# Optimization experiments

Measured on AMD Instinct MI355X. Metric: run time of the kernel, lower is better.

The kernel has to match this reference:

```python
import jax, jax.numpy as jnp
import numpy as np

GROUP_SIZE = 64
SCALING = 32.0 / 16.0  # lora_alpha / r


def setup_inputs() -> dict:
    key = jax.random.key(0)
    k = jax.random.split(key, 7)
    B, S, I, O, R = 4, 2048, 4096, 4096, 16
    G = I // GROUP_SIZE
    x = jax.random.normal(k[0], (B, S, I), dtype=jnp.float32)
    W_q = jax.random.randint(k[1], (O, I), 0, 16, dtype=jnp.int32)
    scale = jax.random.uniform(k[2], (O, G), dtype=jnp.float32) * 0.01 + 1e-4
    zero = jax.random.uniform(k[3], (O, G), dtype=jnp.float32) * 8.0
    lora_A = jax.random.normal(k[4], (I, R), dtype=jnp.float32) * 0.02
    lora_B = jax.random.normal(k[5], (R, O), dtype=jnp.float32) * 0.02
    bias = jax.random.normal(k[6], (O,), dtype=jnp.float32) * 0.01
    return {"x": x, "W_q": W_q, "scale": scale, "zero": zero,
            "lora_A": lora_A, "lora_B": lora_B, "bias": bias}


def reference(x, W_q, scale, zero, lora_A, lora_B, bias):
    O, I = W_q.shape
    G = I // GROUP_SIZE
    # HQQ-style group-wise affine dequant: W = (W_q - zero) * scale  -> [O, I]
    Wg = W_q.reshape(O, G, GROUP_SIZE).astype(scale.dtype)
    W = ((Wg - zero[:, :, None]) * scale[:, :, None]).reshape(O, I)
    # base quantized linear: out = x @ W^T
    out = jnp.einsum('bsi,oi->bso', x, W)
    # LoRA low-rank update (dropout is Identity for p=0)
    out = out + (x @ lora_A @ lora_B) * SCALING
    # bias add
    out = out + bias
    return out
```

## Files before the change

kernel.cpp:

```cpp
#include <hip/hip_runtime.h>
#include <hip/hip_bf16.h>
#include <stdint.h>

#define M_DIM 8192
#define N_DIM 4096
#define K_DIM 4096

typedef __attribute__((ext_vector_type(8))) __bf16 bf16x8;
typedef __attribute__((ext_vector_type(4))) float f32x4;

__device__ inline unsigned short f2bf(float f) {
  unsigned u = __builtin_bit_cast(unsigned, f);
  u += 0x7FFF + ((u >> 16) & 1);
  return (unsigned short)(u >> 16);
}

__device__ inline void async_copy16(const void* g, void* l) {
  __builtin_amdgcn_global_load_lds(
      (const __attribute__((address_space(1))) unsigned int*)g,
      (__attribute__((address_space(3))) unsigned int*)l, 16, 0, 0);
}

__global__ __launch_bounds__(256) void prep_kernel(
    const float* __restrict__ x, unsigned short* __restrict__ xb,
    const int* __restrict__ Wq, const float* __restrict__ scale,
    const float* __restrict__ zero, const float* __restrict__ A,
    const float* __restrict__ Bm, unsigned short* __restrict__ Weff) {
  int t = threadIdx.x;
  if (blockIdx.x < 4096) {
    __shared__ float sA[64 * 17];
    __shared__ float sB[16 * 64];
    int bo = blockIdx.x >> 6;
    int bi = blockIdx.x & 63;
    int o0 = bo * 64, i0 = bi * 64;
    for (int j = t; j < 1024; j += 256) sA[(j >> 4) * 17 + (j & 15)] = A[i0 * 16 + j];
    for (int j = t; j < 1024; j += 256) sB[j] = Bm[(j >> 6) * N_DIM + o0 + (j & 63)];
    __syncthreads();
    for (int e = 0; e < 16; ++e) {
      int idx = e * 256 + t;
      int oo = idx >> 6, ii = idx & 63;
      int o = o0 + oo;
      float sc = scale[o * 64 + bi];
      float zp = zero[o * 64 + bi];
      float w = ((float)Wq[(size_t)o * K_DIM + i0 + ii] - zp) * sc;
      float acc = 0.f;
#pragma unroll
      for (int r = 0; r < 16; ++r) acc += sA[ii * 17 + r] * sB[r * 64 + oo];
      w += 2.0f * acc;
      Weff[(size_t)o * K_DIM + i0 + ii] = f2bf(w);
    }
  } else {
    int i = (blockIdx.x - 4096) * 256 + t;
    int stride = 2048 * 256;
    int n4 = (M_DIM * K_DIM) / 4;
    for (; i < n4; i += stride) {
      float4 v = reinterpret_cast<const float4*>(x)[i];
      ushort4 o;
      o.x = f2bf(v.x); o.y = f2bf(v.y); o.z = f2bf(v.z); o.w = f2bf(v.w);
      reinterpret_cast<ushort4*>(xb)[i] = o;
    }
  }
}

#define BAR() __builtin_amdgcn_s_barrier()
#define SB()  __builtin_amdgcn_sched_barrier(0)
#define WAIT_VM2() do { asm volatile("s_waitcnt vmcnt(2)" ::: "memory"); } while (0)

__device__ __forceinline__ bf16x8 lds_frag(const unsigned short* region, int row, int c) {
  return *reinterpret_cast<const bf16x8*>(region + row * 64 + ((c ^ (row & 7)) << 3));
}

__device__ __forceinline__ void readA(const unsigned short* reg, int mh, int lc, int lr,
                                      bf16x8 a[4][2]) {
#pragma unroll
  for (int m = 0; m < 4; ++m) {
    int row = mh * 64 + m * 16 + lc;
#pragma unroll
    for (int kk = 0; kk < 2; ++kk) a[m][kk] = lds_frag(reg, row, kk * 4 + lr);
  }
}

__device__ __forceinline__ void readB(const unsigned short* reg, int nh, int rB, int lc, int lr,
                                      bf16x8 b[2][2]) {
#pragma unroll
  for (int n = 0; n < 2; ++n) {
    int row = rB + (nh * 2 + n) * 16 + lc;
#pragma unroll
    for (int kk = 0; kk < 2; ++kk) b[n][kk] = lds_frag(reg, row, kk * 4 + lr);
  }
}

__device__ __forceinline__ void mfma_quad(const bf16x8 a[4][2], const bf16x8 b[2][2],
                                          f32x4 acc[8][4], int mh, int nh) {
  __builtin_amdgcn_s_setprio(1);
#pragma unroll
  for (int m = 0; m < 4; ++m)
#pragma unroll
    for (int n = 0; n < 2; ++n)
#pragma unroll
      for (int kk = 0; kk < 2; ++kk)
        acc[mh * 4 + m][nh * 2 + n] = __builtin_amdgcn_mfma_f32_16x16x32_bf16(
            a[m][kk], b[n][kk], acc[mh * 4 + m][nh * 2 + n], 0, 0, 0);
  __builtin_amdgcn_s_setprio(0);
}

__global__ __launch_bounds__(512, 2) void gemm_kernel(
    const unsigned short* __restrict__ xb, const unsigned short* __restrict__ wb,
    const float* __restrict__ bias, float* __restrict__ out) {
  __shared__ unsigned short lds[65536];

  int bid = blockIdx.x;
  int swz = (bid & 7) * 64 + (bid >> 3);
  int mt = swz >> 4, nt = swz & 15;
  int m0 = mt * 256, n0 = nt * 256;

  int tid = threadIdx.x;
  int w = tid >> 6, lane = tid & 63;
  int wr = w >> 2, wc = w & 3;
  int lr = lane >> 4, lc = lane & 15;
  int rB = (wc & 1) * 64;

  int r0 = tid >> 3, c0g = (tid & 7) ^ (r0 & 7);
  int co0 = tid * 8, co1 = (512 + tid) * 8;

  const unsigned short* sA00 = xb + (size_t)(m0 + r0) * K_DIM + c0g * 8;
  const unsigned short* sB00 = wb + (size_t)(n0 + r0) * K_DIM + c0g * 8;

#define STAGE_A(h, buf, kt) do { \
    const unsigned short* _p = sA00 + (size_t)(h) * 128 * K_DIM + (size_t)(kt); \
    async_copy16(_p, &lds[(buf) * 32768 + (h) * 8192 + co0]); \
    async_copy16(_p + (size_t)64 * K_DIM, &lds[(buf) * 32768 + (h) * 8192 + co1]); } while (0)
#define STAGE_B(h, buf, kt) do { \
    const unsigned short* _p = sB00 + (size_t)(h) * 128 * K_DIM + (size_t)(kt); \
    async_copy16(_p, &lds[(buf) * 32768 + 16384 + (h) * 8192 + co0]); \
    async_copy16(_p + (size_t)64 * K_DIM, &lds[(buf) * 32768 + 16384 + (h) * 8192 + co1]); } while (0)

  const unsigned short* aR[2] = { &lds[wr * 8192], &lds[32768 + wr * 8192] };
  const unsigned short* bR[2] = { &lds[16384 + (wc >> 1) * 8192],
                                  &lds[32768 + 16384 + (wc >> 1) * 8192] };

  f32x4 acc[8][4];
#pragma unroll
  for (int i = 0; i < 8; ++i)
#pragma unroll
    for (int j = 0; j < 4; ++j) acc[i][j] = f32x4{0.f, 0.f, 0.f, 0.f};

  STAGE_B(0, 0, 0); STAGE_B(1, 0, 0); STAGE_A(0, 0, 0); STAGE_A(1, 0, 0);
  STAGE_B(0, 1, 64);
  STAGE_B(1, 1, 64); STAGE_A(0, 1, 64);
  asm volatile("s_waitcnt vmcnt(6)" ::: "memory");
  BAR(); SB();

  bf16x8 aU[4][2], aV[4][2], b0[2][2], b1[2][2];
  readA(aR[0], 0, lc, lr, aU); readB(bR[0], 0, rB, lc, lr, b0);
  SB();

#pragma unroll 1
  for (int i = 0; i < 32; ++i) {
    int k1 = (2 * i + 1) * 64;
    int k2 = ((2 * i + 2) & 63) * 64;
    int k3 = ((2 * i + 3) & 63) * 64;

    readB(bR[0], 1, rB, lc, lr, b1);
    SB(); STAGE_A(1, 1, k1); SB();
    mfma_quad(aU, b0, acc, 0, 0);
    SB(); BAR(); SB();
    readA(aR[0], 1, lc, lr, aV);
    SB();
    mfma_quad(aU, b1, acc, 0, 1);
    SB(); BAR(); SB();
    SB(); STAGE_B(0, 0, k2); SB();
    mfma_quad(aV, b0, acc, 1, 0);
    SB(); WAIT_VM2(); BAR(); SB();
    readA(aR[1], 0, lc, lr, aU); readB(bR[1], 0, rB, lc, lr, b0);
    SB(); STAGE_B(1, 0, k2); STAGE_A(0, 0, k2); SB();
    mfma_quad(aV, b1, acc, 1, 1);
    SB(); BAR(); SB();
    readB(bR[1], 1, rB, lc, lr, b1);
    SB(); STAGE_A(1, 0, k2); SB();
    mfma_quad(aU, b0, acc, 0, 0);
    SB(); BAR(); SB();
    readA(aR[1], 1, lc, lr, aV);
    SB();
    mfma_quad(aU, b1, acc, 0, 1);
    SB(); BAR(); SB();
    SB(); STAGE_B(0, 1, k3); SB();
    mfma_quad(aV, b0, acc, 1, 0);
    SB(); WAIT_VM2(); BAR(); SB();
    readA(aR[0], 0, lc, lr, aU); readB(bR[0], 0, rB, lc, lr, b0);
    SB(); STAGE_B(1, 1, k3); STAGE_A(0, 1, k3); SB();
    mfma_quad(aV, b1, acc, 1, 1);
    SB(); BAR(); SB();
  }
  asm volatile("s_waitcnt vmcnt(0) lgkmcnt(0)" ::: "memory");

#pragma unroll
  for (int ni = 0; ni < 4; ++ni) {
    int n = n0 + wc * 64 + ni * 16 + lc;
    float bv = bias[n];
#pragma unroll
    for (int mi = 0; mi < 8; ++mi) {
      int mb = m0 + wr * 128 + mi * 16 + lr * 4;
#pragma unroll
      for (int j = 0; j < 4; ++j)
        out[(size_t)(mb + j) * N_DIM + n] = acc[mi][ni][j] + bv;
    }
  }
#undef STAGE_A
#undef STAGE_B
}

extern "C" void kernel_launch(void* const* d_in, const int* in_sizes, int n_in,
                              void* d_out, int out_size, void* d_ws, size_t ws_size,
                              hipStream_t stream) {
  const float* x     = (const float*)d_in[0];
  const int*   Wq    = (const int*)d_in[1];
  const float* scale = (const float*)d_in[2];
  const float* zero  = (const float*)d_in[3];
  const float* lA    = (const float*)d_in[4];
  const float* lB    = (const float*)d_in[5];
  const float* bias  = (const float*)d_in[6];
  float* out = (float*)d_out;

  unsigned short* xb = (unsigned short*)d_ws;
  unsigned short* wb = (unsigned short*)((char*)d_ws + (size_t)M_DIM * K_DIM * 2);

  prep_kernel<<<6144, 256, 0, stream>>>(x, xb, Wq, scale, zero, lA, lB, wb);
  gemm_kernel<<<512, 512, 0, stream>>>(xb, wb, bias, out);
}
```

Measured before the change: 311.5 us.

## Restructure GEMM main loop into whole-tile stage groups with explicit lgkm waits

```diff
diff --git a/kernel.cpp b/kernel.cpp
--- a/kernel.cpp
+++ b/kernel.cpp
@@ -64,7 +64,9 @@
 
 #define BAR() __builtin_amdgcn_s_barrier()
 #define SB()  __builtin_amdgcn_sched_barrier(0)
-#define WAIT_VM2() do { asm volatile("s_waitcnt vmcnt(2)" ::: "memory"); } while (0)
+#define WAIT_LGKM0() do { asm volatile("s_waitcnt lgkmcnt(0)" ::: "memory"); SB(); } while (0)
+#define HINT_LGKM8() do { asm volatile("s_waitcnt lgkmcnt(8)" ::: "memory"); } while (0)
+#define WAIT_VM8()   do { asm volatile("s_waitcnt vmcnt(8)" ::: "memory"); } while (0)
 
 __device__ __forceinline__ bf16x8 lds_frag(const unsigned short* region, int row, int c) {
   return *reinterpret_cast<const bf16x8*>(region + row * 64 + ((c ^ (row & 7)) << 3));
@@ -146,51 +148,53 @@
     for (int j = 0; j < 4; ++j) acc[i][j] = f32x4{0.f, 0.f, 0.f, 0.f};
 
   STAGE_B(0, 0, 0); STAGE_B(1, 0, 0); STAGE_A(0, 0, 0); STAGE_A(1, 0, 0);
-  STAGE_B(0, 1, 64);
-  STAGE_B(1, 1, 64); STAGE_A(0, 1, 64);
-  asm volatile("s_waitcnt vmcnt(6)" ::: "memory");
+  STAGE_B(0, 1, 64); STAGE_B(1, 1, 64); STAGE_A(0, 1, 64); STAGE_A(1, 1, 64);
+  WAIT_VM8();
   BAR(); SB();
 
   bf16x8 aU[4][2], aV[4][2], b0[2][2], b1[2][2];
-  readA(aR[0], 0, lc, lr, aU); readB(bR[0], 0, rB, lc, lr, b0);
-  SB();
 
 #pragma unroll 1
   for (int i = 0; i < 32; ++i) {
-    int k1 = (2 * i + 1) * 64;
     int k2 = ((2 * i + 2) & 63) * 64;
     int k3 = ((2 * i + 3) & 63) * 64;
 
+    readA(aR[0], 0, lc, lr, aU); readB(bR[0], 0, rB, lc, lr, b0);
+    HINT_LGKM8();
+    SB(); BAR(); WAIT_LGKM0();
+    mfma_quad(aU, b0, acc, 0, 0);
+    SB(); BAR(); SB();
     readB(bR[0], 1, rB, lc, lr, b1);
-    SB(); STAGE_A(1, 1, k1); SB();
+    SB(); BAR(); WAIT_LGKM0();
+    mfma_quad(aU, b1, acc, 0, 1);
+    SB(); BAR(); SB();
+    readA(aR[0], 1, lc, lr, aV);
+    SB(); STAGE_B(0, 0, k2); STAGE_B(1, 0, k2);
+    SB(); BAR(); WAIT_LGKM0();
+    mfma_quad(aV, b1, acc, 1, 1);
+    SB(); BAR(); SB();
+    SB(); STAGE_A(0, 0, k2); STAGE_A(1, 0, k2);
+    SB(); BAR();
+    mfma_quad(aV, b0, acc, 1, 0);
+    SB(); WAIT_VM8(); BAR(); SB();
+    readA(aR[1], 0, lc, lr, aU); readB(bR[1], 0, rB, lc, lr, b0);
+    HINT_LGKM8();
+    SB(); BAR(); WAIT_LGKM0();
     mfma_quad(aU, b0, acc, 0, 0);
     SB(); BAR(); SB();
-    readA(aR[0], 1, lc, lr, aV);
-    SB();
+    readB(bR[1], 1, rB, lc, lr, b1);
+    SB(); BAR(); WAIT_LGKM0();
     mfma_quad(aU, b1, acc, 0, 1);
     SB(); BAR(); SB();
-    SB(); STAGE_B(0, 0, k2); SB();
+    readA(aR[1], 1, lc, lr, aV);
+    SB(); STAGE_B(0, 1, k3); STAGE_B(1, 1, k3);
+    SB(); BAR(); WAIT_LGKM0();
+    mfma_quad(aV, b1, acc, 1, 1);
+    SB(); BAR(); SB();
+    SB(); STAGE_A(0, 1, k3); STAGE_A(1, 1, k3);
+    SB(); BAR();
     mfma_quad(aV, b0, acc, 1, 0);
-    SB(); WAIT_VM2(); BAR(); SB();
-    readA(aR[1], 0, lc, lr, aU); readB(bR[1], 0, rB, lc, lr, b0);
-    SB(); STAGE_B(1, 0, k2); STAGE_A(0, 0, k2); SB();
-    mfma_quad(aV, b1, acc, 1, 1);
-    SB(); BAR(); SB();
-    readB(bR[1], 1, rB, lc, lr, b1);
-    SB(); STAGE_A(1, 0, k2); SB();
-    mfma_quad(aU, b0, acc, 0, 0);
-    SB(); BAR(); SB();
-    readA(aR[1], 1, lc, lr, aV);
-    SB();
-    mfma_quad(aU, b1, acc, 0, 1);
-    SB(); BAR(); SB();
-    SB(); STAGE_B(0, 1, k3); SB();
-    mfma_quad(aV, b0, acc, 1, 0);
-    SB(); WAIT_VM2(); BAR(); SB();
-    readA(aR[0], 0, lc, lr, aU); readB(bR[0], 0, rB, lc, lr, b0);
-    SB(); STAGE_B(1, 1, k3); STAGE_A(0, 1, k3); SB();
-    mfma_quad(aV, b1, acc, 1, 1);
-    SB(); BAR(); SB();
+    SB(); WAIT_VM8(); BAR(); SB();
   }
   asm volatile("s_waitcnt vmcnt(0) lgkmcnt(0)" ::: "memory");
 
```

New measurement: 325.1 us. +4.3%, slower.
